# Performance work log

Hardware: AMD Instinct MI355X
Metric: run time of the kernel (lower is better)

## Reference

```python
import jax, jax.numpy as jnp
import numpy as np

N_NODES = 100000
N_EDGES = 1600000
IN_DIM, HID_DIM, OUT_DIM = 256, 128, 128


def gcn_norm(edge_index, edge_weight, num_nodes):
    # Add self-loops with weight 1 (PyG GCNConv default fill_value=1.0)
    loop = jnp.arange(num_nodes, dtype=edge_index.dtype)
    src = jnp.concatenate([edge_index[0], loop])
    dst = jnp.concatenate([edge_index[1], loop])
    w = jnp.concatenate([edge_weight, jnp.ones((num_nodes,), edge_weight.dtype)])
    # Symmetric normalization: deg computed at destination over edge weights
    deg = jax.ops.segment_sum(w, dst, num_segments=num_nodes)
    dinv = jnp.where(deg > 0, jax.lax.rsqrt(deg), 0.0)
    norm = dinv[src] * w * dinv[dst]  # [E + N]
    return src, dst, norm


def gcn_conv(x, W, b, src, dst, norm, num_nodes):
    h = x @ W                                  # [N, out]
    msg = h[src] * norm[:, None]               # gather + scale, [E+N, out]
    out = jax.ops.segment_sum(msg, dst, num_segments=num_nodes)  # scatter-add
    return out + b


def setup_inputs() -> dict:
    key = jax.random.key(0)
    ks = jax.random.split(key, 8)
    x = jax.random.normal(ks[0], (N_NODES, IN_DIM), dtype=jnp.float32)
    edge_index = jax.random.randint(ks[1], (2, N_EDGES), 0, N_NODES, dtype=jnp.int64)
    edge_weight = jax.random.uniform(ks[2], (N_EDGES,), dtype=jnp.float32)
    s1 = 1.0 / np.sqrt(IN_DIM)
    s2 = 1.0 / np.sqrt(HID_DIM)
    W1 = jax.random.uniform(ks[3], (IN_DIM, HID_DIM), jnp.float32, -s1, s1)
    b1 = jnp.zeros((HID_DIM,), jnp.float32)
    W2 = jax.random.uniform(ks[4], (HID_DIM, OUT_DIM), jnp.float32, -s2, s2)
    b2 = jnp.zeros((OUT_DIM,), jnp.float32)
    return {"x": x, "edge_index": edge_index, "edge_weight": edge_weight,
            "W1": W1, "b1": b1, "W2": W2, "b2": b2}


def reference(x, edge_index, edge_weight, W1, b1, W2, b2):
    n = x.shape[0]
    src, dst, norm = gcn_norm(edge_index, edge_weight, n)
    h = jax.nn.relu(gcn_conv(x, W1, b1, src, dst, norm, n))
    out = gcn_conv(h, W2, b2, src, dst, norm, n)
    return out
```

## Files before the change

kernel.cpp:

```cpp
#include <hip/hip_runtime.h>
#include <stdint.h>

#define N_NODES 100000
#define N_EDGES 1600000
#define IN_DIM 256
#define HID_DIM 128
#define OUT_DIM 128

#define NBUCK 391
#define CHUNK 4096

typedef __attribute__((ext_vector_type(8))) short short8;
typedef __attribute__((ext_vector_type(4))) float floatx4;

__device__ __forceinline__ float bf2f(unsigned short u) {
    union { unsigned int i; float f; } v; v.i = ((unsigned int)u) << 16; return v.f;
}
__device__ __forceinline__ unsigned short f2bf(float f) {
    union { float fl; unsigned int i; } v; v.fl = f;
    unsigned int x = v.i;
    return (unsigned short)((x + 0x7fffu + ((x >> 16) & 1u)) >> 16);
}
__device__ __forceinline__ float bflo(unsigned int u) {
    union { unsigned int i; float f; } v; v.i = u << 16; return v.f;
}
__device__ __forceinline__ float bfhi(unsigned int u) {
    union { unsigned int i; float f; } v; v.i = u & 0xffff0000u; return v.f;
}
__device__ __forceinline__ float asf(unsigned int u) {
    union { unsigned int i; float f; } v; v.i = u; return v.f;
}
__device__ __forceinline__ unsigned int asu(float f) {
    union { float fl; unsigned int i; } v; v.fl = f; return v.i;
}

__global__ void k_detect(const unsigned int* __restrict__ xu, const unsigned int* __restrict__ eu,
                         int* __restrict__ flags) {
    __shared__ int s_huge, s_odd;
    if (threadIdx.x == 0) { s_huge = 0; s_odd = 0; }
    __syncthreads();
    int huge = 0, odd = 0;
    for (int i = threadIdx.x; i < 1024; i += 256) {
        unsigned int b = xu[i];
        unsigned int e = (b >> 23) & 0xffu;
        if (e >= 0xf0u) huge = 1;
        if (eu[2 * i + 1] != 0) odd = 1;
    }
    if (huge) atomicOr(&s_huge, 1);
    if (odd) atomicOr(&s_odd, 1);
    __syncthreads();
    if (threadIdx.x == 0) { flags[0] = s_huge ? 0 : 1; flags[1] = s_odd ? 0 : 1; }
}

__device__ __forceinline__ int load_idx(const void* base, long long i, int i64m) {
    int v = i64m ? (int)((const long long*)base)[i] : ((const int*)base)[i];
    return v < 0 ? 0 : (v >= N_NODES ? N_NODES - 1 : v);
}
__device__ __forceinline__ float load_f(const void* base, long long i, int f32m) {
    return f32m ? ((const float*)base)[i] : bf2f(((const unsigned short*)base)[i]);
}

__global__ void k_zero(int* bucket_cnt) {
    int t = threadIdx.x;
    if (t < NBUCK) bucket_cnt[t] = 0;
}

__global__ void k_bhist(const void* __restrict__ ei, const int* __restrict__ flags,
                        int* __restrict__ bucket_cnt, int e) {
    __shared__ int h[NBUCK];
    for (int t = threadIdx.x; t < NBUCK; t += 256) h[t] = 0;
    __syncthreads();
    int i64m = flags[1];
    int base = blockIdx.x * CHUNK;
    int end = base + CHUNK < e ? base + CHUNK : e;
    for (int i = base + threadIdx.x; i < end; i += 256) {
        int d = load_idx(ei, (long long)N_EDGES + i, i64m);
        atomicAdd(&h[d >> 8], 1);
    }
    __syncthreads();
    for (int t = threadIdx.x; t < NBUCK; t += 256)
        if (h[t]) atomicAdd(&bucket_cnt[t], h[t]);
}

__global__ void k_bscan(const int* __restrict__ bucket_cnt, int* __restrict__ bucket_base,
                        int* __restrict__ bucket_cursor, int* __restrict__ rowptr) {
    __shared__ int lds[512];
    int t = threadIdx.x;
    int v = (t < NBUCK) ? bucket_cnt[t] : 0;
    lds[t] = v;
    __syncthreads();
    for (int off = 1; off < 512; off <<= 1) {
        int x = (t >= off) ? lds[t - off] : 0;
        __syncthreads();
        lds[t] += x;
        __syncthreads();
    }
    int excl = lds[t] - v;
    if (t < NBUCK) { bucket_base[t] = excl; bucket_cursor[t] = excl; }
    if (t == 0) { bucket_base[NBUCK] = lds[NBUCK - 1]; rowptr[N_NODES] = N_EDGES; }
}

__global__ void k_bscatter(const void* __restrict__ ei, const void* __restrict__ ew,
                           const int* __restrict__ flags, int* __restrict__ bucket_cursor,
                           uint2* __restrict__ ebuf, int e) {
    __shared__ int h[NBUCK];
    for (int t = threadIdx.x; t < NBUCK; t += 256) h[t] = 0;
    __syncthreads();
    int f32m = flags[0], i64m = flags[1];
    int base = blockIdx.x * CHUNK;
    int end = base + CHUNK < e ? base + CHUNK : e;
    for (int i = base + threadIdx.x; i < end; i += 256) {
        int d = load_idx(ei, (long long)N_EDGES + i, i64m);
        atomicAdd(&h[d >> 8], 1);
    }
    __syncthreads();
    for (int t = threadIdx.x; t < NBUCK; t += 256) {
        int c = h[t];
        h[t] = c ? atomicAdd(&bucket_cursor[t], c) : 0;
    }
    __syncthreads();
    for (int i = base + threadIdx.x; i < end; i += 256) {
        int s = load_idx(ei, i, i64m);
        int d = load_idx(ei, (long long)N_EDGES + i, i64m);
        float w = load_f(ew, i, f32m);
        int b = d >> 8;
        int p = atomicAdd(&h[b], 1);
        uint2 c; c.x = (unsigned int)s | ((unsigned int)(d & 255) << 17); c.y = asu(w);
        ebuf[p] = c;
    }
}

__global__ void k_fine(const uint2* __restrict__ ebuf, const int* __restrict__ bucket_base,
                       uint2* __restrict__ csr, int* __restrict__ rowptr,
                       float* __restrict__ dinv, int n) {
    __shared__ int h[256];
    __shared__ float fw[256];
    __shared__ int c2[256];
    int t = threadIdx.x, b = blockIdx.x;
    int e0 = bucket_base[b], e1 = bucket_base[b + 1];
    h[t] = 0; fw[t] = 0.f;
    __syncthreads();
    for (int i = e0 + t; i < e1; i += 256) {
        uint2 c = ebuf[i];
        int dl = (c.x >> 17) & 255;
        atomicAdd(&h[dl], 1);
        atomicAdd(&fw[dl], asf(c.y));
    }
    __syncthreads();
    int own = h[t];
    for (int off = 1; off < 256; off <<= 1) {
        int x = (t >= off) ? h[t - off] : 0;
        __syncthreads();
        h[t] += x;
        __syncthreads();
    }
    int excl = h[t] - own;
    int node = (b << 8) + t;
    if (node < n) {
        rowptr[node] = e0 + excl;
        dinv[node] = rsqrtf(1.0f + fw[t]);
    }
    c2[t] = e0 + excl;
    __syncthreads();
    for (int i = e0 + t; i < e1; i += 256) {
        uint2 c = ebuf[i];
        int dl = (c.x >> 17) & 255;
        int p = atomicAdd(&c2[dl], 1);
        csr[p] = c;
    }
}

__global__ void k_norm(uint2* __restrict__ csr, const float* __restrict__ dinv, int e) {
    int i = blockIdx.x * 256 + threadIdx.x;
    if (i < e) {
        uint2 c = csr[i];
        csr[i].y = asu(asf(c.y) * dinv[c.x & 0x1FFFF]);
    }
}

__global__ void k_transpose(const void* __restrict__ W1, const void* __restrict__ W2,
                            const int* __restrict__ flags,
                            unsigned short* __restrict__ W1T, unsigned short* __restrict__ W2T) {
    int i = blockIdx.x * 256 + threadIdx.x;
    int f32m = flags[0];
    if (i < IN_DIM * HID_DIM) {
        int k = i / HID_DIM, n = i % HID_DIM;
        W1T[n * IN_DIM + k] = f2bf(load_f(W1, i, f32m));
    } else {
        int j = i - IN_DIM * HID_DIM;
        if (j < HID_DIM * OUT_DIM) {
            int k = j / OUT_DIM, n = j % OUT_DIM;
            W2T[n * HID_DIM + k] = f2bf(load_f(W2, j, f32m));
        }
    }
}

template <int K, bool RAWA>
__global__ void k_gemm(const void* __restrict__ A, const unsigned short* __restrict__ WT,
                       unsigned short* __restrict__ H, const int* __restrict__ flags, int n) {
    int wave = threadIdx.x >> 6;
    int lane = threadIdx.x & 63;
    int quad = lane >> 4;
    int l16 = lane & 15;
    int rowbase = blockIdx.x * 64 + wave * 16;
    int arow = rowbase + l16;
    if (arow >= n) arow = n - 1;
    int f32m = RAWA ? flags[0] : 0;

    floatx4 acc[8];
#pragma unroll
    for (int c = 0; c < 8; c++) acc[c] = (floatx4){0.f, 0.f, 0.f, 0.f};

#pragma unroll
    for (int k0 = 0; k0 < K; k0 += 32) {
        short8 af;
        if (RAWA && f32m) {
            const float* ap = (const float*)A + (size_t)arow * K + quad * 8 + k0;
            float4 u0 = *(const float4*)ap;
            float4 u1 = *(const float4*)(ap + 4);
            af[0] = (short)f2bf(u0.x); af[1] = (short)f2bf(u0.y);
            af[2] = (short)f2bf(u0.z); af[3] = (short)f2bf(u0.w);
            af[4] = (short)f2bf(u1.x); af[5] = (short)f2bf(u1.y);
            af[6] = (short)f2bf(u1.z); af[7] = (short)f2bf(u1.w);
        } else {
            af = *(const short8*)((const unsigned short*)A + (size_t)arow * K + quad * 8 + k0);
        }
#pragma unroll
        for (int c = 0; c < 8; c++) {
            const unsigned short* bptr = WT + (size_t)(c * 16 + l16) * K + k0 + quad * 8;
            short8 bf = *(const short8*)bptr;
            acc[c] = __builtin_amdgcn_mfma_f32_16x16x32_bf16(af, bf, acc[c], 0, 0, 0);
        }
    }

#pragma unroll
    for (int c = 0; c < 8; c++) {
#pragma unroll
        for (int r = 0; r < 4; r++) {
            int grow = rowbase + quad * 4 + r;
            if (grow < n) H[(size_t)grow * 128 + c * 16 + l16] = f2bf(acc[c][r]);
        }
    }
}

template <bool RELU, bool FINAL>
__global__ void k_aggregate(const unsigned short* __restrict__ H, const int* __restrict__ rowptr,
                            const uint2* __restrict__ csr, const float* __restrict__ dinv,
                            const void* __restrict__ bias, void* __restrict__ out,
                            const int* __restrict__ flags, int n) {
    int node = blockIdx.x * 8 + (threadIdx.x >> 5);
    int lane = threadIdx.x & 31;
    if (node >= n) return;
    int col = lane * 4;
    int f32m = flags[0];

    float a0 = 0.f, a1 = 0.f, a2 = 0.f, a3 = 0.f;
    int e0 = rowptr[node], e1 = rowptr[node + 1];
    int e = e0;
    for (; e + 2 <= e1; e += 2) {
        uint2 c0 = csr[e], c1 = csr[e + 1];
        uint2 h0 = *(const uint2*)(H + (size_t)(c0.x & 0x1FFFF) * 128 + col);
        uint2 h1 = *(const uint2*)(H + (size_t)(c1.x & 0x1FFFF) * 128 + col);
        float w0 = asf(c0.y), w1 = asf(c1.y);
        a0 += w0 * bflo(h0.x); a1 += w0 * bfhi(h0.x);
        a2 += w0 * bflo(h0.y); a3 += w0 * bfhi(h0.y);
        a0 += w1 * bflo(h1.x); a1 += w1 * bfhi(h1.x);
        a2 += w1 * bflo(h1.y); a3 += w1 * bfhi(h1.y);
    }
    if (e < e1) {
        uint2 c0 = csr[e];
        uint2 h0 = *(const uint2*)(H + (size_t)(c0.x & 0x1FFFF) * 128 + col);
        float w0 = asf(c0.y);
        a0 += w0 * bflo(h0.x); a1 += w0 * bfhi(h0.x);
        a2 += w0 * bflo(h0.y); a3 += w0 * bfhi(h0.y);
    }

    float dn = dinv[node];
    float coef = dn * dn;
    uint2 u = *(const uint2*)(H + (size_t)node * 128 + col);
    a0 = dn * a0 + coef * bflo(u.x) + load_f(bias, col, f32m);
    a1 = dn * a1 + coef * bfhi(u.x) + load_f(bias, col + 1, f32m);
    a2 = dn * a2 + coef * bflo(u.y) + load_f(bias, col + 2, f32m);
    a3 = dn * a3 + coef * bfhi(u.y) + load_f(bias, col + 3, f32m);

    if (RELU) {
        a0 = fmaxf(a0, 0.f); a1 = fmaxf(a1, 0.f);
        a2 = fmaxf(a2, 0.f); a3 = fmaxf(a3, 0.f);
    }
    if (FINAL && f32m) {
        float4 o = {a0, a1, a2, a3};
        *(float4*)((float*)out + (size_t)node * 128 + col) = o;
    } else {
        uint2 o;
        o.x = (unsigned int)f2bf(a0) | ((unsigned int)f2bf(a1) << 16);
        o.y = (unsigned int)f2bf(a2) | ((unsigned int)f2bf(a3) << 16);
        *(uint2*)((unsigned short*)out + (size_t)node * 128 + col) = o;
    }
}

extern "C" void kernel_launch(void* const* d_in, const int* in_sizes, int n_in,
                              void* d_out, int out_size, void* d_ws, size_t ws_size,
                              hipStream_t stream) {
    const void* x  = d_in[0];
    const void* ei = d_in[1];
    const void* ew = d_in[2];
    const void* W1 = d_in[3];
    const void* b1 = d_in[4];
    const void* W2 = d_in[5];
    const void* b2 = d_in[6];

    char* p = (char*)d_ws;
    auto alloc = [&](size_t bytes) { char* r = p; p += (bytes + 255) & ~(size_t)255; return r; };
    int*   flags    = (int*)alloc(256);
    float* dinv     = (float*)alloc((size_t)N_NODES * 4);
    int*   rowptr   = (int*)alloc((size_t)(N_NODES + 1) * 4);
    int*   bucket_cnt    = (int*)alloc((size_t)NBUCK * 4);
    int*   bucket_base   = (int*)alloc((size_t)(NBUCK + 1) * 4);
    int*   bucket_cursor = (int*)alloc((size_t)NBUCK * 4);
    uint2* csr      = (uint2*)alloc((size_t)N_EDGES * 8);
    unsigned short* W1T  = (unsigned short*)alloc((size_t)IN_DIM * HID_DIM * 2);
    unsigned short* W2T  = (unsigned short*)alloc((size_t)HID_DIM * OUT_DIM * 2);
    unsigned short* hbuf = (unsigned short*)alloc((size_t)N_NODES * 128 * 2);
    unsigned short* zbuf = (unsigned short*)alloc((size_t)N_NODES * 128 * 2);
    uint2* ebuf = (uint2*)hbuf;

    int nbE = (N_EDGES + 255) / 256;
    int nbC = (N_EDGES + CHUNK - 1) / CHUNK;

    k_detect<<<1, 256, 0, stream>>>((const unsigned int*)x, (const unsigned int*)ei, flags);
    k_zero<<<1, 512, 0, stream>>>(bucket_cnt);
    k_bhist<<<nbC, 256, 0, stream>>>(ei, flags, bucket_cnt, N_EDGES);
    k_bscan<<<1, 512, 0, stream>>>(bucket_cnt, bucket_base, bucket_cursor, rowptr);
    k_bscatter<<<nbC, 256, 0, stream>>>(ei, ew, flags, bucket_cursor, ebuf, N_EDGES);
    k_fine<<<NBUCK, 256, 0, stream>>>(ebuf, bucket_base, csr, rowptr, dinv, N_NODES);
    k_norm<<<nbE, 256, 0, stream>>>(csr, dinv, N_EDGES);
    k_transpose<<<(IN_DIM * HID_DIM + HID_DIM * OUT_DIM + 255) / 256, 256, 0, stream>>>(W1, W2, flags, W1T, W2T);

    k_gemm<IN_DIM, true><<<(N_NODES + 63) / 64, 256, 0, stream>>>(x, W1T, hbuf, flags, N_NODES);
    k_aggregate<true, false><<<(N_NODES + 7) / 8, 256, 0, stream>>>(hbuf, rowptr, csr, dinv,
                                                                    b1, zbuf, flags, N_NODES);
    k_gemm<HID_DIM, false><<<(N_NODES + 63) / 64, 256, 0, stream>>>(zbuf, W2T, hbuf, flags, N_NODES);
    k_aggregate<false, true><<<(N_NODES + 7) / 8, 256, 0, stream>>>(hbuf, rowptr, csr, dinv,
                                                                    b2, d_out, flags, N_NODES);
}
```

Measured before the change: 492.6 us.

## Stage weights in swizzled LDS, double row tiles and prefetch in GEMM; unroll aggregation

The GEMM now loads the transposed weight matrix into shared memory with an XOR-style swizzle to avoid bank conflicts. Each wave computes two 16-row tiles that reuse the same B fragment, and the next A chunk is prefetched in registers. The aggregation loop is unrolled to four edges per iteration for more memory-level parallelism, and the bucket-zero kernel is folded into the detect kernel to save a launch. The trade-offs are more LDS use per block (64KB for K=256), which lowers occupancy, and higher register pressure.

```diff
diff --git a/kernel.cpp b/kernel.cpp
--- a/kernel.cpp
+++ b/kernel.cpp
@@ -33,14 +33,29 @@
 __device__ __forceinline__ unsigned int asu(float f) {
     union { float fl; unsigned int i; } v; v.fl = f; return v.i;
 }
+__device__ __forceinline__ unsigned int pack2(float a, float b) {
+    unsigned int ua = asu(a), ub = asu(b);
+    ua += 0x7fffu + ((ua >> 16) & 1u);
+    ub += 0x7fffu + ((ub >> 16) & 1u);
+    return (ua >> 16) | (ub & 0xffff0000u);
+}
+__device__ __forceinline__ short8 pack8(float4 a, float4 b) {
+    union { unsigned int u[4]; short8 s; } r;
+    r.u[0] = pack2(a.x, a.y);
+    r.u[1] = pack2(a.z, a.w);
+    r.u[2] = pack2(b.x, b.y);
+    r.u[3] = pack2(b.z, b.w);
+    return r.s;
+}
 
 __global__ void k_detect(const unsigned int* __restrict__ xu, const unsigned int* __restrict__ eu,
-                         int* __restrict__ flags) {
+                         int* __restrict__ flags, int* __restrict__ bucket_cnt) {
     __shared__ int s_huge, s_odd;
     if (threadIdx.x == 0) { s_huge = 0; s_odd = 0; }
+    if (threadIdx.x < NBUCK) bucket_cnt[threadIdx.x] = 0;
     __syncthreads();
     int huge = 0, odd = 0;
-    for (int i = threadIdx.x; i < 1024; i += 256) {
+    for (int i = threadIdx.x; i < 1024; i += 512) {
         unsigned int b = xu[i];
         unsigned int e = (b >> 23) & 0xffu;
         if (e >= 0xf0u) huge = 1;
@@ -58,11 +73,6 @@
 }
 __device__ __forceinline__ float load_f(const void* base, long long i, int f32m) {
     return f32m ? ((const float*)base)[i] : bf2f(((const unsigned short*)base)[i]);
-}
-
-__global__ void k_zero(int* bucket_cnt) {
-    int t = threadIdx.x;
-    if (t < NBUCK) bucket_cnt[t] = 0;
 }
 
 __global__ void k_bhist(const void* __restrict__ ei, const int* __restrict__ flags,
@@ -195,52 +205,114 @@
     }
 }
 
+template <int K, bool F32M>
+__device__ __forceinline__ void gemm_loop(const void* __restrict__ A,
+                                          const unsigned short* __restrict__ Bs,
+                                          size_t aoff0, size_t aoff1,
+                                          int quad, int l16, floatx4 (&acc)[2][8]) {
+    constexpr int NCH = K / 32;
+    constexpr int BMASK = K / 8 - 1;
+    float4 fraw[2][2];
+    short8 braw[2];
+    if (F32M) {
+        const float* ap = (const float*)A;
+        fraw[0][0] = *(const float4*)(ap + aoff0);
+        fraw[0][1] = *(const float4*)(ap + aoff0 + 4);
+        fraw[1][0] = *(const float4*)(ap + aoff1);
+        fraw[1][1] = *(const float4*)(ap + aoff1 + 4);
+    } else {
+        const unsigned short* ap = (const unsigned short*)A;
+        braw[0] = *(const short8*)(ap + aoff0);
+        braw[1] = *(const short8*)(ap + aoff1);
+    }
+#pragma unroll
+    for (int ch = 0; ch < NCH; ch++) {
+        float4 nf[2][2];
+        short8 nb[2];
+        if (ch + 1 < NCH) {
+            int o = (ch + 1) * 32;
+            if (F32M) {
+                const float* ap = (const float*)A;
+                nf[0][0] = *(const float4*)(ap + aoff0 + o);
+                nf[0][1] = *(const float4*)(ap + aoff0 + o + 4);
+                nf[1][0] = *(const float4*)(ap + aoff1 + o);
+                nf[1][1] = *(const float4*)(ap + aoff1 + o + 4);
+            } else {
+                const unsigned short* ap = (const unsigned short*)A;
+                nb[0] = *(const short8*)(ap + aoff0 + o);
+                nb[1] = *(const short8*)(ap + aoff1 + o);
+            }
+        }
+        short8 a0, a1;
+        if (F32M) {
+            a0 = pack8(fraw[0][0], fraw[0][1]);
+            a1 = pack8(fraw[1][0], fraw[1][1]);
+        } else {
+            a0 = braw[0];
+            a1 = braw[1];
+        }
+#pragma unroll
+        for (int c = 0; c < 8; c++) {
+            int col = c * 16 + l16;
+            int boff = col * K + 8 * ((ch * 4 + quad + (col & 7)) & BMASK);
+            short8 bf = *(const short8*)(Bs + boff);
+            acc[0][c] = __builtin_amdgcn_mfma_f32_16x16x32_bf16(a0, bf, acc[0][c], 0, 0, 0);
+            acc[1][c] = __builtin_amdgcn_mfma_f32_16x16x32_bf16(a1, bf, acc[1][c], 0, 0, 0);
+        }
+        if (ch + 1 < NCH) {
+            if (F32M) {
+                fraw[0][0] = nf[0][0]; fraw[0][1] = nf[0][1];
+                fraw[1][0] = nf[1][0]; fraw[1][1] = nf[1][1];
+            } else {
+                braw[0] = nb[0]; braw[1] = nb[1];
+            }
+        }
+    }
+}
+
 template <int K, bool RAWA>
 __global__ void k_gemm(const void* __restrict__ A, const unsigned short* __restrict__ WT,
                        unsigned short* __restrict__ H, const int* __restrict__ flags, int n) {
+    __shared__ unsigned short Bs[128 * K];
+    for (int base = threadIdx.x * 8; base < 128 * K; base += 256 * 8) {
+        int col = base / K;
+        int k = base - col * K;
+        int ks = (k + (col & 7) * 8) & (K - 1);
+        *(short8*)(&Bs[col * K + ks]) = *(const short8*)(WT + base);
+    }
+    __syncthreads();
+
     int wave = threadIdx.x >> 6;
     int lane = threadIdx.x & 63;
     int quad = lane >> 4;
     int l16 = lane & 15;
-    int rowbase = blockIdx.x * 64 + wave * 16;
-    int arow = rowbase + l16;
-    if (arow >= n) arow = n - 1;
+    int rowbase = blockIdx.x * 128 + wave * 32;
+    int r0 = rowbase + l16;        if (r0 >= n) r0 = n - 1;
+    int r1 = rowbase + 16 + l16;   if (r1 >= n) r1 = n - 1;
+    size_t aoff0 = (size_t)r0 * K + quad * 8;
+    size_t aoff1 = (size_t)r1 * K + quad * 8;
+
+    floatx4 acc[2][8];
+#pragma unroll
+    for (int t = 0; t < 2; t++)
+#pragma unroll
+        for (int c = 0; c < 8; c++) acc[t][c] = (floatx4){0.f, 0.f, 0.f, 0.f};
+
     int f32m = RAWA ? flags[0] : 0;
-
-    floatx4 acc[8];
-#pragma unroll
-    for (int c = 0; c < 8; c++) acc[c] = (floatx4){0.f, 0.f, 0.f, 0.f};
-
-#pragma unroll
-    for (int k0 = 0; k0 < K; k0 += 32) {
-        short8 af;
-        if (RAWA && f32m) {
-            const float* ap = (const float*)A + (size_t)arow * K + quad * 8 + k0;
-            float4 u0 = *(const float4*)ap;
-            float4 u1 = *(const float4*)(ap + 4);
-            af[0] = (short)f2bf(u0.x); af[1] = (short)f2bf(u0.y);
-            af[2] = (short)f2bf(u0.z); af[3] = (short)f2bf(u0.w);
-            af[4] = (short)f2bf(u1.x); af[5] = (short)f2bf(u1.y);
-            af[6] = (short)f2bf(u1.z); af[7] = (short)f2bf(u1.w);
-        } else {
-            af = *(const short8*)((const unsigned short*)A + (size_t)arow * K + quad * 8 + k0);
-        }
-#pragma unroll
-        for (int c = 0; c < 8; c++) {
-            const unsigned short* bptr = WT + (size_t)(c * 16 + l16) * K + k0 + quad * 8;
-            short8 bf = *(const short8*)bptr;
-            acc[c] = __builtin_amdgcn_mfma_f32_16x16x32_bf16(af, bf, acc[c], 0, 0, 0);
-        }
-    }
-
-#pragma unroll
-    for (int c = 0; c < 8; c++) {
-#pragma unroll
-        for (int r = 0; r < 4; r++) {
-            int grow = rowbase + quad * 4 + r;
-            if (grow < n) H[(size_t)grow * 128 + c * 16 + l16] = f2bf(acc[c][r]);
-        }
-    }
+    if (RAWA && f32m)
+        gemm_loop<K, true>(A, Bs, aoff0, aoff1, quad, l16, acc);
+    else
+        gemm_loop<K, false>(A, Bs, aoff0, aoff1, quad, l16, acc);
+
+#pragma unroll
+    for (int t = 0; t < 2; t++)
+#pragma unroll
+        for (int c = 0; c < 8; c++)
+#pragma unroll
+            for (int r = 0; r < 4; r++) {
+                int grow = rowbase + t * 16 + quad * 4 + r;
+                if (grow < n) H[(size_t)grow * 128 + c * 16 + l16] = f2bf(acc[t][c][r]);
+            }
 }
 
 template <bool RELU, bool FINAL>
@@ -257,17 +329,19 @@
     float a0 = 0.f, a1 = 0.f, a2 = 0.f, a3 = 0.f;
     int e0 = rowptr[node], e1 = rowptr[node + 1];
     int e = e0;
-    for (; e + 2 <= e1; e += 2) {
-        uint2 c0 = csr[e], c1 = csr[e + 1];
+    for (; e + 4 <= e1; e += 4) {
+        uint2 c0 = csr[e], c1 = csr[e + 1], c2 = csr[e + 2], c3 = csr[e + 3];
         uint2 h0 = *(const uint2*)(H + (size_t)(c0.x & 0x1FFFF) * 128 + col);
         uint2 h1 = *(const uint2*)(H + (size_t)(c1.x & 0x1FFFF) * 128 + col);
-        float w0 = asf(c0.y), w1 = asf(c1.y);
-        a0 += w0 * bflo(h0.x); a1 += w0 * bfhi(h0.x);
-        a2 += w0 * bflo(h0.y); a3 += w0 * bfhi(h0.y);
-        a0 += w1 * bflo(h1.x); a1 += w1 * bfhi(h1.x);
-        a2 += w1 * bflo(h1.y); a3 += w1 * bfhi(h1.y);
-    }
-    if (e < e1) {
+        uint2 h2 = *(const uint2*)(H + (size_t)(c2.x & 0x1FFFF) * 128 + col);
+        uint2 h3 = *(const uint2*)(H + (size_t)(c3.x & 0x1FFFF) * 128 + col);
+        float w0 = asf(c0.y), w1 = asf(c1.y), w2 = asf(c2.y), w3 = asf(c3.y);
+        a0 += w0 * bflo(h0.x); a1 += w0 * bfhi(h0.x); a2 += w0 * bflo(h0.y); a3 += w0 * bfhi(h0.y);
+        a0 += w1 * bflo(h1.x); a1 += w1 * bfhi(h1.x); a2 += w1 * bflo(h1.y); a3 += w1 * bfhi(h1.y);
+        a0 += w2 * bflo(h2.x); a1 += w2 * bfhi(h2.x); a2 += w2 * bflo(h2.y); a3 += w2 * bfhi(h2.y);
+        a0 += w3 * bflo(h3.x); a1 += w3 * bfhi(h3.x); a2 += w3 * bflo(h3.y); a3 += w3 * bfhi(h3.y);
+    }
+    for (; e < e1; e++) {
         uint2 c0 = csr[e];
         uint2 h0 = *(const uint2*)(H + (size_t)(c0.x & 0x1FFFF) * 128 + col);
         float w0 = asf(c0.y);
@@ -326,9 +400,9 @@
 
     int nbE = (N_EDGES + 255) / 256;
     int nbC = (N_EDGES + CHUNK - 1) / CHUNK;
-
-    k_detect<<<1, 256, 0, stream>>>((const unsigned int*)x, (const unsigned int*)ei, flags);
-    k_zero<<<1, 512, 0, stream>>>(bucket_cnt);
+    int nbG = (N_NODES + 127) / 128;
+
+    k_detect<<<1, 512, 0, stream>>>((const unsigned int*)x, (const unsigned int*)ei, flags, bucket_cnt);
     k_bhist<<<nbC, 256, 0, stream>>>(ei, flags, bucket_cnt, N_EDGES);
     k_bscan<<<1, 512, 0, stream>>>(bucket_cnt, bucket_base, bucket_cursor, rowptr);
     k_bscatter<<<nbC, 256, 0, stream>>>(ei, ew, flags, bucket_cursor, ebuf, N_EDGES);
@@ -336,10 +410,10 @@
     k_norm<<<nbE, 256, 0, stream>>>(csr, dinv, N_EDGES);
     k_transpose<<<(IN_DIM * HID_DIM + HID_DIM * OUT_DIM + 255) / 256, 256, 0, stream>>>(W1, W2, flags, W1T, W2T);
 
-    k_gemm<IN_DIM, true><<<(N_NODES + 63) / 64, 256, 0, stream>>>(x, W1T, hbuf, flags, N_NODES);
+    k_gemm<IN_DIM, true><<<nbG, 256, 0, stream>>>(x, W1T, hbuf, flags, N_NODES);
     k_aggregate<true, false><<<(N_NODES + 7) / 8, 256, 0, stream>>>(hbuf, rowptr, csr, dinv,
                                                                     b1, zbuf, flags, N_NODES);
-    k_gemm<HID_DIM, false><<<(N_NODES + 63) / 64, 256, 0, stream>>>(zbuf, W2T, hbuf, flags, N_NODES);
+    k_gemm<HID_DIM, false><<<nbG, 256, 0, stream>>>(zbuf, W2T, hbuf, flags, N_NODES);
     k_aggregate<false, true><<<(N_NODES + 7) / 8, 256, 0, stream>>>(hbuf, rowptr, csr, dinv,
                                                                     b2, d_out, flags, N_NODES);
 }
```

Result: faster. 437.6 us (-11.2%).
